# Kernel optimization log

Hardware: AMD Instinct MI355X
Metric: run time of the kernel (lower is better)

## Reference

```python
import jax, jax.numpy as jnp
import numpy as np

T, DIM, AH, HID, E = 2048, 1024, 2048, 1024, 8
N_HEADS, HEAD_DIM = 16, 128
N_GROUPS, TOPK_GROUPS, TOPK = 4, 2, 1
ROUTE_SCALE = 1.0


def rmsnorm(x, w, eps=1e-6):
    xf = x.astype(jnp.float32)
    var = jnp.mean(xf * xf, axis=-1, keepdims=True)
    return (xf * jax.lax.rsqrt(var + eps)).astype(x.dtype) * w


def setup_inputs() -> dict:
    key = jax.random.key(0)
    ks = jax.random.split(key, 12)

    def xavier(k, fan_in, fan_out, gain=1.0):
        lim = gain * np.sqrt(6.0 / (fan_in + fan_out))
        return jax.random.uniform(k, (fan_in, fan_out), minval=-lim, maxval=lim, dtype=jnp.float32)

    return {
        "x": jax.random.normal(ks[0], (T, DIM), dtype=jnp.float32),
        "x_projected": jax.random.normal(ks[1], (T, AH), dtype=jnp.float32),
        "attn_norm_w": jnp.ones((AH,), dtype=jnp.float32),
        # stored as [in, out] (transposed vs torch Linear)
        "wq": 0.02 * jax.random.normal(ks[2], (AH, N_HEADS * HEAD_DIM), dtype=jnp.float32),
        "bq": jnp.zeros((N_HEADS * HEAD_DIM,), dtype=jnp.float32),
        "wk": 0.02 * jax.random.normal(ks[3], (AH, N_HEADS * HEAD_DIM), dtype=jnp.float32),
        "bk": jnp.zeros((N_HEADS * HEAD_DIM,), dtype=jnp.float32),
        "q_norm_w": jnp.ones((HEAD_DIM,), dtype=jnp.float32),
        "k_norm_w": jnp.ones((HEAD_DIM,), dtype=jnp.float32),
        "w1": xavier(ks[4], DIM, HID),
        "b1": jnp.zeros((HID,), dtype=jnp.float32),
        "w2": xavier(ks[5], HID, HID),
        "b2": jnp.zeros((HID,), dtype=jnp.float32),
        "w3": xavier(ks[6], HID, E, gain=0.1),
        "b3": jnp.zeros((E,), dtype=jnp.float32),
    }


def reference(x, x_projected, attn_norm_w, wq, bq, wk, bk, q_norm_w, k_norm_w,
              w1, b1, w2, b2, w3, b3):
    t = x.shape[0]
    # ---- attention probe (torch.no_grad -> stop_gradient) ----
    xn = rmsnorm(x_projected, attn_norm_w)                      # [T, AH]
    q = (xn @ wq + bq).reshape(t, N_HEADS, HEAD_DIM)
    k = (xn @ wk + bk).reshape(t, N_HEADS, HEAD_DIM)
    q = rmsnorm(q, q_norm_w)
    k = rmsnorm(k, k_norm_w)
    scores = jnp.einsum('qhd,khd->hqk', q, k) / np.float32(np.sqrt(HEAD_DIM))
    probs = jax.nn.softmax(scores, axis=-1)                     # [H, T, T]
    # sum over query axis, mean over heads -> attention received per token
    importance = jax.lax.stop_gradient(probs.sum(axis=1).mean(axis=0))  # [T]

    # ---- router MLP (eval mode: dropout = identity) ----
    h = jax.nn.gelu(x @ w1 + b1, approximate=False)
    h = jax.nn.gelu(h @ w2 + b2, approximate=False)
    logits = h @ w3 + b3                                        # [T, E]
    r_scores = jax.nn.softmax(logits, axis=-1)

    # ---- grouped top-k (group-limited top-1 routing) ----
    sg = r_scores.reshape(t, N_GROUPS, E // N_GROUPS)
    group_scores = sg.max(axis=-1)                              # [T, G]
    _, gidx = jax.lax.top_k(group_scores, TOPK_GROUPS)          # [T, kg]
    mask = jnp.zeros((t, N_GROUPS), dtype=bool).at[jnp.arange(t)[:, None], gidx].set(True)
    masked = jnp.where(mask[:, :, None], sg, -jnp.inf).reshape(t, E)
    _, idx = jax.lax.top_k(masked, TOPK)                        # [T, 1]
    weights = jnp.take_along_axis(r_scores, idx, axis=1) * ROUTE_SCALE  # [T, 1]
    return weights, idx, importance
```

## Files before the change

### kernel.cpp

```cpp
#include <hip/hip_runtime.h>

#define T_TOK 2048
#define DIMX  1024
#define AHX   2048
#define HIDX  1024
#define NEXP  8
#define NHEAD 16
#define HD    128

typedef short bf16x8 __attribute__((ext_vector_type(8)));
typedef float f32x4  __attribute__((ext_vector_type(4)));

__device__ __forceinline__ unsigned short f2bf(float f){
  unsigned int u = __builtin_bit_cast(unsigned int, f);
  u += 0x7FFFu + ((u >> 16) & 1u);
  return (unsigned short)(u >> 16);
}
__device__ __forceinline__ float bf2f(unsigned short h){
  unsigned int u = ((unsigned int)h) << 16;
  return __builtin_bit_cast(float, u);
}
__device__ __forceinline__ float gelu_exact(float x){
  return 0.5f * x * (1.0f + erff(x * 0.70710678118654752440f));
}
__device__ __forceinline__ void gload16(const unsigned short* g, unsigned short* l){
  __builtin_amdgcn_global_load_lds((const __attribute__((address_space(1))) unsigned int*)g,
                                   (__attribute__((address_space(3))) unsigned int*)l, 16, 0, 0);
}

__global__ __launch_bounds__(256) void k_prep(const float* __restrict__ x,
                                              unsigned short* __restrict__ xh,
                                              unsigned short* __restrict__ xl,
                                              const float* __restrict__ xproj,
                                              const float* __restrict__ anw,
                                              unsigned short* __restrict__ xn){
  int bx = blockIdx.x, t = threadIdx.x;
  if (bx < 8192){
    int i = bx * 256 + t;
    float v = x[i];
    unsigned short h = f2bf(v);
    xh[i] = h;
    xl[i] = f2bf(v - bf2f(h));
    return;
  }
  int row = bx - 8192;
  const float* p = xproj + (size_t)row * AHX;
  float v[8];
  *(float4*)&v[0] = *(const float4*)(p + t * 8);
  *(float4*)&v[4] = *(const float4*)(p + t * 8 + 4);
  float s = 0.f;
  #pragma unroll
  for (int i = 0; i < 8; i++) s += v[i] * v[i];
  #pragma unroll
  for (int m = 1; m < 64; m <<= 1) s += __shfl_xor(s, m);
  __shared__ float ps[4];
  if ((t & 63) == 0) ps[t >> 6] = s;
  __syncthreads();
  float tot = ps[0] + ps[1] + ps[2] + ps[3];
  float rs = rsqrtf(tot * (1.0f / AHX) + 1e-6f);
  #pragma unroll
  for (int i = 0; i < 8; i++)
    xn[(size_t)row * AHX + t * 8 + i] = f2bf(v[i] * rs * anw[t * 8 + i]);
}

__global__ void k_transpose_qk(const float* __restrict__ wq, const float* __restrict__ wk,
                               unsigned short* __restrict__ out){
  const float* in = blockIdx.z ? wk : wq;
  unsigned short* o = out + (size_t)blockIdx.z * AHX * AHX;
  __shared__ float tile[32][33];
  int bx = blockIdx.x * 32, by = blockIdx.y * 32;
  int tx = threadIdx.x, ty = threadIdx.y;
  #pragma unroll
  for (int i = 0; i < 32; i += 8)
    tile[ty + i][tx] = in[(size_t)(by + ty + i) * AHX + bx + tx];
  __syncthreads();
  #pragma unroll
  for (int i = 0; i < 32; i += 8)
    o[(size_t)(bx + ty + i) * AHX + by + tx] = f2bf(tile[tx][ty + i]);
}

__global__ void k_transpose_w12(const float* __restrict__ w1, const float* __restrict__ w2,
                                unsigned short* __restrict__ w1h, unsigned short* __restrict__ w1l,
                                unsigned short* __restrict__ w2h, unsigned short* __restrict__ w2l){
  const float* in = blockIdx.z ? w2 : w1;
  unsigned short* oh = blockIdx.z ? w2h : w1h;
  unsigned short* ol = blockIdx.z ? w2l : w1l;
  __shared__ float tile[32][33];
  int bx = blockIdx.x * 32, by = blockIdx.y * 32;
  int tx = threadIdx.x, ty = threadIdx.y;
  #pragma unroll
  for (int i = 0; i < 32; i += 8)
    tile[ty + i][tx] = in[(size_t)(by + ty + i) * HIDX + bx + tx];
  __syncthreads();
  #pragma unroll
  for (int i = 0; i < 32; i += 8){
    float v = tile[tx][ty + i];
    unsigned short h = f2bf(v);
    size_t o = (size_t)(bx + ty + i) * DIMX + by + tx;
    oh[o] = h;
    ol[o] = f2bf(v - bf2f(h));
  }
}

__global__ __launch_bounds__(256) void k_gemm_qk(
    const unsigned short* __restrict__ A, const unsigned short* __restrict__ B,
    const float* __restrict__ bq, const float* __restrict__ bk,
    const float* __restrict__ qnw, const float* __restrict__ knw,
    unsigned short* __restrict__ Qnn, unsigned short* __restrict__ Knn, int K)
{
  __shared__ __align__(16) unsigned short sA[2][128 * 64];
  __shared__ __align__(16) unsigned short sB[2][128 * 64];
  __shared__ float sums[128][2];
  int tid = threadIdx.x;
  int bm = blockIdx.y * 128;
  int bnB = blockIdx.x * 128;
  int w = tid >> 6, l = tid & 63;
  int wm = (w >> 1) * 64, wn = (w & 1) * 64;
  int lhi = l >> 4, llo = l & 15;
  int srow = l >> 3;
  int scol = ((l & 7) ^ srow) * 8;
  int swz = llo & 7;

  const unsigned short* pA = &A[(size_t)(bm + w * 32 + srow) * K + scol];
  const unsigned short* pB = &B[(size_t)(bnB + w * 32 + srow) * K + scol];

  f32x4 acc[4][4] = {};

  #pragma unroll
  for (int i = 0; i < 4; i++){
    gload16(pA + (size_t)i * 8 * K, &sA[0][(w * 32 + i * 8) * 64]);
    gload16(pB + (size_t)i * 8 * K, &sB[0][(w * 32 + i * 8) * 64]);
  }
  __syncthreads();

  int cur = 0;
  for (int k0 = 0; k0 < K; k0 += 64){
    if (k0 + 64 < K){
      #pragma unroll
      for (int i = 0; i < 4; i++){
        gload16(pA + (size_t)i * 8 * K + k0 + 64, &sA[cur ^ 1][(w * 32 + i * 8) * 64]);
        gload16(pB + (size_t)i * 8 * K + k0 + 64, &sB[cur ^ 1][(w * 32 + i * 8) * 64]);
      }
    }
    bf16x8 af[2][4], bfr[2][4];
    #pragma unroll
    for (int kk = 0; kk < 2; kk++){
      int ca = ((kk * 4 + lhi) ^ swz) * 8;
      #pragma unroll
      for (int m = 0; m < 4; m++){
        af[kk][m]  = *(const bf16x8*)&sA[cur][(wm + m * 16 + llo) * 64 + ca];
        bfr[kk][m] = *(const bf16x8*)&sB[cur][(wn + m * 16 + llo) * 64 + ca];
      }
    }
    #pragma unroll
    for (int kk = 0; kk < 2; kk++)
      #pragma unroll
      for (int m = 0; m < 4; m++)
        #pragma unroll
        for (int n = 0; n < 4; n++)
          acc[m][n] = __builtin_amdgcn_mfma_f32_16x16x32_bf16(af[kk][m], bfr[kk][n], acc[m][n], 0, 0, 0);
    __syncthreads();
    cur ^= 1;
  }

  bool isq = blockIdx.x < 16;
  const float* bias = isq ? bq : bk;
  const float* nw   = isq ? qnw : knw;
  unsigned short* outp = isq ? Qnn : Knn;
  int hcol0 = (blockIdx.x & 15) * 128;

  #pragma unroll
  for (int n = 0; n < 4; n++){
    float bv = bias[hcol0 + wn + n * 16 + llo];
    #pragma unroll
    for (int m = 0; m < 4; m++)
      #pragma unroll
      for (int j = 0; j < 4; j++) acc[m][n][j] += bv;
  }
  #pragma unroll
  for (int m = 0; m < 4; m++)
    #pragma unroll
    for (int j = 0; j < 4; j++){
      float p = 0.f;
      #pragma unroll
      for (int n = 0; n < 4; n++) p += acc[m][n][j] * acc[m][n][j];
      p += __shfl_xor(p, 1); p += __shfl_xor(p, 2);
      p += __shfl_xor(p, 4); p += __shfl_xor(p, 8);
      if (llo == 0) sums[wm + m * 16 + lhi * 4 + j][w & 1] = p;
    }
  __syncthreads();
  #pragma unroll
  for (int m = 0; m < 4; m++)
    #pragma unroll
    for (int j = 0; j < 4; j++){
      int row = wm + m * 16 + lhi * 4 + j;
      float rs = rsqrtf((sums[row][0] + sums[row][1]) * (1.0f / HD) + 1e-6f);
      #pragma unroll
      for (int n = 0; n < 4; n++){
        int col = wn + n * 16 + llo;
        outp[(size_t)(bm + row) * AHX + hcol0 + col] = f2bf(acc[m][n][j] * rs * nw[col]);
      }
    }
}

template<int EPI>
__global__ __launch_bounds__(256) void k_gemm_mlp(
    const unsigned short* __restrict__ Ah_, const unsigned short* __restrict__ Al_,
    const unsigned short* __restrict__ Bh_, const unsigned short* __restrict__ Bl_,
    const float* __restrict__ bias,
    float* __restrict__ Cf, unsigned short* __restrict__ Ch, unsigned short* __restrict__ Cl,
    int N, int K)
{
  __shared__ __align__(16) unsigned short sAh[2][64 * 64], sAl[2][64 * 64];
  __shared__ __align__(16) unsigned short sBh[2][64 * 64], sBl[2][64 * 64];
  int tid = threadIdx.x;
  int bm = blockIdx.y * 64, bn = blockIdx.x * 64;
  int w = tid >> 6, l = tid & 63;
  int wm = (w >> 1) * 32, wn = (w & 1) * 32;
  int lhi = l >> 4, llo = l & 15;
  int srow = l >> 3;
  int scol = ((l & 7) ^ srow) * 8;
  int swz = llo & 7;

  const unsigned short* pAh = &Ah_[(size_t)(bm + w * 8 + srow) * K + scol];
  const unsigned short* pAl = &Al_[(size_t)(bm + w * 8 + srow) * K + scol];
  const unsigned short* pBh = &Bh_[(size_t)(bn + w * 8 + srow) * K + scol];
  const unsigned short* pBl = &Bl_[(size_t)(bn + w * 8 + srow) * K + scol];

  f32x4 acc[2][2] = {};

  auto stage = [&](int buf, int k0){
    #pragma unroll
    for (int i = 0; i < 2; i++){
      int rb = (i * 32 + w * 8) * 64;
      gload16(pAh + (size_t)i * 32 * K + k0, &sAh[buf][rb]);
      gload16(pAl + (size_t)i * 32 * K + k0, &sAl[buf][rb]);
      gload16(pBh + (size_t)i * 32 * K + k0, &sBh[buf][rb]);
      gload16(pBl + (size_t)i * 32 * K + k0, &sBl[buf][rb]);
    }
  };

  stage(0, 0);
  __syncthreads();

  int cur = 0;
  for (int k0 = 0; k0 < K; k0 += 64){
    if (k0 + 64 < K) stage(cur ^ 1, k0 + 64);
    bf16x8 ah[2][2], al[2][2], bh[2][2], bl[2][2];
    #pragma unroll
    for (int kk = 0; kk < 2; kk++){
      int ca = ((kk * 4 + lhi) ^ swz) * 8;
      #pragma unroll
      for (int m = 0; m < 2; m++){
        ah[kk][m] = *(const bf16x8*)&sAh[cur][(wm + m * 16 + llo) * 64 + ca];
        al[kk][m] = *(const bf16x8*)&sAl[cur][(wm + m * 16 + llo) * 64 + ca];
        bh[kk][m] = *(const bf16x8*)&sBh[cur][(wn + m * 16 + llo) * 64 + ca];
        bl[kk][m] = *(const bf16x8*)&sBl[cur][(wn + m * 16 + llo) * 64 + ca];
      }
    }
    #pragma unroll
    for (int kk = 0; kk < 2; kk++)
      #pragma unroll
      for (int m = 0; m < 2; m++)
        #pragma unroll
        for (int n = 0; n < 2; n++){
          acc[m][n] = __builtin_amdgcn_mfma_f32_16x16x32_bf16(ah[kk][m], bh[kk][n], acc[m][n], 0, 0, 0);
          acc[m][n] = __builtin_amdgcn_mfma_f32_16x16x32_bf16(ah[kk][m], bl[kk][n], acc[m][n], 0, 0, 0);
          acc[m][n] = __builtin_amdgcn_mfma_f32_16x16x32_bf16(al[kk][m], bh[kk][n], acc[m][n], 0, 0, 0);
        }
    __syncthreads();
    cur ^= 1;
  }

  #pragma unroll
  for (int m = 0; m < 2; m++)
    #pragma unroll
    for (int n = 0; n < 2; n++){
      int col = bn + wn + n * 16 + llo;
      float bv = bias[col];
      #pragma unroll
      for (int j = 0; j < 4; j++){
        int row = bm + wm + m * 16 + lhi * 4 + j;
        float v = acc[m][n][j] + bv;
        size_t off = (size_t)row * N + col;
        if constexpr (EPI == 1){
          float g = gelu_exact(v);
          unsigned short hh = f2bf(g);
          Ch[off] = hh;
          Cl[off] = f2bf(g - bf2f(hh));
        } else {
          Cf[off] = gelu_exact(v);
        }
      }
    }
}

__global__ __launch_bounds__(256) void k_z(const unsigned short* __restrict__ Qn,
                                           const unsigned short* __restrict__ Kn,
                                           float* __restrict__ zpart){
  __shared__ __align__(16) unsigned short sK[2][128 * 128];
  int h = blockIdx.y;
  int qb = blockIdx.x * 128;
  int tid = threadIdx.x, w = tid >> 6, l = tid & 63;
  int lhi = l >> 4, llo = l & 15;
  int wq = qb + w * 32;
  const float scale = 0.08838834764831845f;

  auto stageK = [&](int buf, int kt){
    #pragma unroll
    for (int i = 0; i < 8; i++){
      int rb = i * 16 + w * 4;
      int r = rb + (l >> 4);
      int c = ((l & 15) * 8) ^ ((r & 7) << 3);
      gload16(&Kn[(size_t)(kt + r) * AHX + h * HD + c], &sK[buf][rb * 128]);
    }
  };

  bf16x8 qf[2][4];
  #pragma unroll
  for (int m = 0; m < 2; m++)
    #pragma unroll
    for (int kk = 0; kk < 4; kk++)
      qf[m][kk] = *(const bf16x8*)&Qn[(size_t)(wq + m * 16 + llo) * AHX + h * HD + kk * 32 + lhi * 8];

  float rz[2][4] = {};
  int kt0 = blockIdx.z * 256;

  stageK(0, kt0);
  __syncthreads();

  #pragma unroll
  for (int t = 0; t < 2; t++){
    if (t == 0) stageK(1, kt0 + 128);
    f32x4 acc[2][8] = {};
    #pragma unroll
    for (int n = 0; n < 8; n++){
      int row = n * 16 + llo;
      #pragma unroll
      for (int kk = 0; kk < 4; kk++){
        bf16x8 kf = *(const bf16x8*)&sK[t][row * 128 + ((kk * 32 + lhi * 8) ^ ((llo & 7) << 3))];
        acc[0][n] = __builtin_amdgcn_mfma_f32_16x16x32_bf16(qf[0][kk], kf, acc[0][n], 0, 0, 0);
        acc[1][n] = __builtin_amdgcn_mfma_f32_16x16x32_bf16(qf[1][kk], kf, acc[1][n], 0, 0, 0);
      }
    }
    #pragma unroll
    for (int m = 0; m < 2; m++)
      #pragma unroll
      for (int j = 0; j < 4; j++){
        float s = 0.f;
        #pragma unroll
        for (int n = 0; n < 8; n++) s += __expf(acc[m][n][j] * scale);
        rz[m][j] += s;
      }
    if (t == 0) __syncthreads();
  }
  #pragma unroll
  for (int m = 0; m < 2; m++)
    #pragma unroll
    for (int j = 0; j < 4; j++){
      float s = rz[m][j];
      s += __shfl_xor(s, 1); s += __shfl_xor(s, 2);
      s += __shfl_xor(s, 4); s += __shfl_xor(s, 8);
      if (llo == 0){
        int row = wq + m * 16 + lhi * 4 + j;
        zpart[(size_t)blockIdx.z * (NHEAD * T_TOK) + h * T_TOK + row] = s;
      }
    }
}

__global__ void k_rc(const float* __restrict__ zpart, float* __restrict__ rc){
  int i = blockIdx.x * 256 + threadIdx.x;
  float s = 0.f;
  #pragma unroll
  for (int p = 0; p < 8; p++) s += zpart[p * (NHEAD * T_TOK) + i];
  rc[i] = 1.0f / ((float)NHEAD * s);
}

__global__ __launch_bounds__(256) void k_imp(const unsigned short* __restrict__ Qn,
                                             const unsigned short* __restrict__ Kn,
                                             const float* __restrict__ rc,
                                             float* __restrict__ imp_part){
  __shared__ __align__(16) unsigned short sK[2][128 * 128];
  __shared__ float simp[4][128];
  int h = blockIdx.y;
  int qb = blockIdx.x * 128;
  int kt0 = blockIdx.z * 256;
  int tid = threadIdx.x, w = tid >> 6, l = tid & 63;
  int lhi = l >> 4, llo = l & 15;
  int wq = qb + w * 32;
  const float scale = 0.08838834764831845f;

  auto stageK = [&](int buf, int kt){
    #pragma unroll
    for (int i = 0; i < 8; i++){
      int rb = i * 16 + w * 4;
      int r = rb + (l >> 4);
      int c = ((l & 15) * 8) ^ ((r & 7) << 3);
      gload16(&Kn[(size_t)(kt + r) * AHX + h * HD + c], &sK[buf][rb * 128]);
    }
  };

  bf16x8 qf[2][4];
  float rcv[2][4];
  #pragma unroll
  for (int m = 0; m < 2; m++)
    #pragma unroll
    for (int kk = 0; kk < 4; kk++)
      qf[m][kk] = *(const bf16x8*)&Qn[(size_t)(wq + m * 16 + llo) * AHX + h * HD + kk * 32 + lhi * 8];
  #pragma unroll
  for (int m = 0; m < 2; m++)
    #pragma unroll
    for (int j = 0; j < 4; j++)
      rcv[m][j] = rc[h * T_TOK + wq + m * 16 + lhi * 4 + j];

  stageK(0, kt0);
  __syncthreads();

  #pragma unroll
  for (int t = 0; t < 2; t++){
    if (t == 0) stageK(1, kt0 + 128);
    f32x4 acc[2][8] = {};
    #pragma unroll
    for (int n = 0; n < 8; n++){
      int row = n * 16 + llo;
      #pragma unroll
      for (int kk = 0; kk < 4; kk++){
        bf16x8 kf = *(const bf16x8*)&sK[t][row * 128 + ((kk * 32 + lhi * 8) ^ ((llo & 7) << 3))];
        acc[0][n] = __builtin_amdgcn_mfma_f32_16x16x32_bf16(qf[0][kk], kf, acc[0][n], 0, 0, 0);
        acc[1][n] = __builtin_amdgcn_mfma_f32_16x16x32_bf16(qf[1][kk], kf, acc[1][n], 0, 0, 0);
      }
    }
    #pragma unroll
    for (int n = 0; n < 8; n++){
      float s = 0.f;
      #pragma unroll
      for (int m = 0; m < 2; m++)
        #pragma unroll
        for (int j = 0; j < 4; j++)
          s += __expf(acc[m][j / 4 * 0 + n][j] * 0.f + acc[m][n][j] * scale) * 0.f + __expf(acc[m][n][j] * scale) * rcv[m][j];
      s += __shfl_xor(s, 16);
      s += __shfl_xor(s, 32);
      if (l < 16) simp[w][n * 16 + l] = s;
    }
    __syncthreads();
    if (tid < 128){
      float tot = simp[0][tid] + simp[1][tid] + simp[2][tid] + simp[3][tid];
      imp_part[((size_t)blockIdx.x * NHEAD + h) * T_TOK + kt0 + t * 128 + tid] = tot;
    }
    if (t == 0) __syncthreads();
  }
}

__global__ __launch_bounds__(256) void k_final(const float* __restrict__ imp_part,
                                               const float* __restrict__ h2,
                                               const float* __restrict__ w3,
                                               const float* __restrict__ b3,
                                               float* __restrict__ out){
  if (blockIdx.x < 8){
    int col = blockIdx.x * 256 + threadIdx.x;
    float s = 0.f;
    for (int r = 0; r < 256; r++) s += imp_part[(size_t)r * T_TOK + col];
    out[2 * T_TOK + col] = s;
    return;
  }
  int t = (blockIdx.x - 8) * 4 + (threadIdx.x >> 6);
  int l = threadIdx.x & 63;
  const float* hp = h2 + (size_t)t * HIDX;
  float acc[NEXP] = {};
  for (int i = l; i < HIDX; i += 64){
    float hv = hp[i];
    const float* wr = w3 + (size_t)i * NEXP;
    #pragma unroll
    for (int e = 0; e < NEXP; e++) acc[e] = fmaf(hv, wr[e], acc[e]);
  }
  #pragma unroll
  for (int mk = 1; mk < 64; mk <<= 1)
    #pragma unroll
    for (int e = 0; e < NEXP; e++) acc[e] += __shfl_xor(acc[e], mk);
  if (l == 0){
    float lg[NEXP], mx = -__builtin_inff();
    #pragma unroll
    for (int e = 0; e < NEXP; e++){ lg[e] = acc[e] + b3[e]; mx = fmaxf(mx, lg[e]); }
    float Z = 0.f, p[NEXP];
    #pragma unroll
    for (int e = 0; e < NEXP; e++){ p[e] = expf(lg[e] - mx); Z += p[e]; }
    float invZ = 1.0f / Z;
    #pragma unroll
    for (int e = 0; e < NEXP; e++) p[e] *= invZ;
    float gs[4];
    #pragma unroll
    for (int g = 0; g < 4; g++) gs[g] = fmaxf(p[2 * g], p[2 * g + 1]);
    int g1 = 0;
    #pragma unroll
    for (int g = 1; g < 4; g++) if (gs[g] > gs[g1]) g1 = g;
    int g2 = -1; float g2v = -__builtin_inff();
    #pragma unroll
    for (int g = 0; g < 4; g++) if (g != g1 && gs[g] > g2v){ g2v = gs[g]; g2 = g; }
    int best = 0; float bv = -__builtin_inff();
    #pragma unroll
    for (int e = 0; e < NEXP; e++){
      int g = e >> 1;
      if ((g == g1 || g == g2) && p[e] > bv){ bv = p[e]; best = e; }
    }
    out[t]         = bv;
    out[T_TOK + t] = (float)best;
  }
}

extern "C" void kernel_launch(void* const* d_in, const int* in_sizes, int n_in,
                              void* d_out, int out_size, void* d_ws, size_t ws_size,
                              hipStream_t stream){
  const float* x     = (const float*)d_in[0];
  const float* xproj = (const float*)d_in[1];
  const float* anw   = (const float*)d_in[2];
  const float* wq    = (const float*)d_in[3];
  const float* bq    = (const float*)d_in[4];
  const float* wk    = (const float*)d_in[5];
  const float* bk    = (const float*)d_in[6];
  const float* qnw   = (const float*)d_in[7];
  const float* knw   = (const float*)d_in[8];
  const float* w1    = (const float*)d_in[9];
  const float* b1    = (const float*)d_in[10];
  const float* w2    = (const float*)d_in[11];
  const float* b2    = (const float*)d_in[12];
  const float* w3    = (const float*)d_in[13];
  const float* b3    = (const float*)d_in[14];
  float* out = (float*)d_out;

  char* ws = (char*)d_ws;
  const size_t MB = 1024 * 1024;
  unsigned short* xn   = (unsigned short*)(ws);
  unsigned short* wqkT = (unsigned short*)(ws + 8 * MB);
  unsigned short* Qnn  = (unsigned short*)(ws + 24 * MB);
  unsigned short* Knn  = (unsigned short*)(ws + 32 * MB);
  float* zpart         = (float*)(ws + 40 * MB);
  float* rc            = (float*)(ws + 41 * MB);
  float* imp_part      = (float*)(ws + 42 * MB);
  unsigned short* xh   = (unsigned short*)(ws + 44 * MB);
  unsigned short* xl   = (unsigned short*)(ws + 48 * MB);
  unsigned short* w1Th = (unsigned short*)(ws + 52 * MB);
  unsigned short* w1Tl = (unsigned short*)(ws + 54 * MB);
  unsigned short* w2Th = (unsigned short*)(ws + 56 * MB);
  unsigned short* w2Tl = (unsigned short*)(ws + 58 * MB);
  unsigned short* h1h  = (unsigned short*)(ws + 60 * MB);
  unsigned short* h1l  = (unsigned short*)(ws + 64 * MB);
  float* h2            = (float*)(ws + 68 * MB);

  dim3 tb(32, 8);
  k_prep<<<8192 + T_TOK, 256, 0, stream>>>(x, xh, xl, xproj, anw, xn);
  k_transpose_qk<<<dim3(AHX / 32, AHX / 32, 2), tb, 0, stream>>>(wq, wk, wqkT);

  k_gemm_qk<<<dim3(32, 16), 256, 0, stream>>>(xn, wqkT, bq, bk, qnw, knw, Qnn, Knn, AHX);

  k_transpose_w12<<<dim3(HIDX / 32, DIMX / 32, 2), tb, 0, stream>>>(w1, w2, w1Th, w1Tl, w2Th, w2Tl);

  k_z<<<dim3(16, NHEAD, 8), 256, 0, stream>>>(Qnn, Knn, zpart);
  k_rc<<<(NHEAD * T_TOK) / 256, 256, 0, stream>>>(zpart, rc);
  k_imp<<<dim3(16, NHEAD, 8), 256, 0, stream>>>(Qnn, Knn, rc, imp_part);

  k_gemm_mlp<1><<<dim3(HIDX / 64, T_TOK / 64), 256, 0, stream>>>(
      xh, xl, w1Th, w1Tl, b1, nullptr, h1h, h1l, HIDX, DIMX);
  k_gemm_mlp<2><<<dim3(HIDX / 64, T_TOK / 64), 256, 0, stream>>>(
      h1h, h1l, w2Th, w2Tl, b2, h2, nullptr, nullptr, HIDX, HIDX);

  k_final<<<8 + T_TOK / 4, 256, 0, stream>>>(imp_part, h2, w3, b3, out);

  (void)in_sizes; (void)n_in; (void)out_size; (void)ws_size;
}
```

Measured before the change: 194.5 us.

## Merge prep/transpose kernels, fold rc into imp, use 512-thread blocks for attention GEMMs

Merges the prep and both weight-transpose kernels into one launch, and folds the k_rc normalization into k_imp so it reads zpart directly. It also doubles block size to 512 threads for the QK projection, z and importance kernels, so each wave holds a smaller tile and fewer accumulators. The intent is to cut launch count and raise occupancy and latency hiding. The cost is less register reuse per wave, redundant zpart reads in k_imp, and an extra barrier per iteration.

```diff
diff --git a/kernel.cpp b/kernel.cpp
--- a/kernel.cpp
+++ b/kernel.cpp
@@ -8,128 +8,136 @@
 #define NHEAD 16
 #define HD    128
 
+typedef unsigned short us;
 typedef short bf16x8 __attribute__((ext_vector_type(8)));
 typedef float f32x4  __attribute__((ext_vector_type(4)));
 
-__device__ __forceinline__ unsigned short f2bf(float f){
+__device__ __forceinline__ us f2bf(float f){
   unsigned int u = __builtin_bit_cast(unsigned int, f);
   u += 0x7FFFu + ((u >> 16) & 1u);
-  return (unsigned short)(u >> 16);
-}
-__device__ __forceinline__ float bf2f(unsigned short h){
+  return (us)(u >> 16);
+}
+__device__ __forceinline__ float bf2f(us h){
   unsigned int u = ((unsigned int)h) << 16;
   return __builtin_bit_cast(float, u);
 }
 __device__ __forceinline__ float gelu_exact(float x){
   return 0.5f * x * (1.0f + erff(x * 0.70710678118654752440f));
 }
-__device__ __forceinline__ void gload16(const unsigned short* g, unsigned short* l){
+__device__ __forceinline__ void gload16(const us* g, us* l){
   __builtin_amdgcn_global_load_lds((const __attribute__((address_space(1))) unsigned int*)g,
                                    (__attribute__((address_space(3))) unsigned int*)l, 16, 0, 0);
 }
 
-__global__ __launch_bounds__(256) void k_prep(const float* __restrict__ x,
-                                              unsigned short* __restrict__ xh,
-                                              unsigned short* __restrict__ xl,
-                                              const float* __restrict__ xproj,
-                                              const float* __restrict__ anw,
-                                              unsigned short* __restrict__ xn){
+__global__ __launch_bounds__(256) void k_pre(const float* __restrict__ x,
+                                             us* __restrict__ xh, us* __restrict__ xl,
+                                             const float* __restrict__ xproj,
+                                             const float* __restrict__ anw,
+                                             us* __restrict__ xn,
+                                             const float* __restrict__ wq,
+                                             const float* __restrict__ wk,
+                                             us* __restrict__ wqkT,
+                                             const float* __restrict__ w1,
+                                             const float* __restrict__ w2,
+                                             us* __restrict__ w1h, us* __restrict__ w1l,
+                                             us* __restrict__ w2h, us* __restrict__ w2l){
+  __shared__ float tile[32][33];
+  __shared__ float ps[4];
   int bx = blockIdx.x, t = threadIdx.x;
   if (bx < 8192){
     int i = bx * 256 + t;
     float v = x[i];
-    unsigned short h = f2bf(v);
+    us h = f2bf(v);
     xh[i] = h;
     xl[i] = f2bf(v - bf2f(h));
     return;
   }
-  int row = bx - 8192;
-  const float* p = xproj + (size_t)row * AHX;
-  float v[8];
-  *(float4*)&v[0] = *(const float4*)(p + t * 8);
-  *(float4*)&v[4] = *(const float4*)(p + t * 8 + 4);
-  float s = 0.f;
-  #pragma unroll
-  for (int i = 0; i < 8; i++) s += v[i] * v[i];
-  #pragma unroll
-  for (int m = 1; m < 64; m <<= 1) s += __shfl_xor(s, m);
-  __shared__ float ps[4];
-  if ((t & 63) == 0) ps[t >> 6] = s;
-  __syncthreads();
-  float tot = ps[0] + ps[1] + ps[2] + ps[3];
-  float rs = rsqrtf(tot * (1.0f / AHX) + 1e-6f);
-  #pragma unroll
-  for (int i = 0; i < 8; i++)
-    xn[(size_t)row * AHX + t * 8 + i] = f2bf(v[i] * rs * anw[t * 8 + i]);
-}
-
-__global__ void k_transpose_qk(const float* __restrict__ wq, const float* __restrict__ wk,
-                               unsigned short* __restrict__ out){
-  const float* in = blockIdx.z ? wk : wq;
-  unsigned short* o = out + (size_t)blockIdx.z * AHX * AHX;
-  __shared__ float tile[32][33];
-  int bx = blockIdx.x * 32, by = blockIdx.y * 32;
-  int tx = threadIdx.x, ty = threadIdx.y;
-  #pragma unroll
-  for (int i = 0; i < 32; i += 8)
-    tile[ty + i][tx] = in[(size_t)(by + ty + i) * AHX + bx + tx];
-  __syncthreads();
-  #pragma unroll
-  for (int i = 0; i < 32; i += 8)
-    o[(size_t)(bx + ty + i) * AHX + by + tx] = f2bf(tile[tx][ty + i]);
-}
-
-__global__ void k_transpose_w12(const float* __restrict__ w1, const float* __restrict__ w2,
-                                unsigned short* __restrict__ w1h, unsigned short* __restrict__ w1l,
-                                unsigned short* __restrict__ w2h, unsigned short* __restrict__ w2l){
-  const float* in = blockIdx.z ? w2 : w1;
-  unsigned short* oh = blockIdx.z ? w2h : w1h;
-  unsigned short* ol = blockIdx.z ? w2l : w1l;
-  __shared__ float tile[32][33];
-  int bx = blockIdx.x * 32, by = blockIdx.y * 32;
-  int tx = threadIdx.x, ty = threadIdx.y;
-  #pragma unroll
-  for (int i = 0; i < 32; i += 8)
-    tile[ty + i][tx] = in[(size_t)(by + ty + i) * HIDX + bx + tx];
-  __syncthreads();
-  #pragma unroll
-  for (int i = 0; i < 32; i += 8){
-    float v = tile[tx][ty + i];
-    unsigned short h = f2bf(v);
-    size_t o = (size_t)(bx + ty + i) * DIMX + by + tx;
-    oh[o] = h;
-    ol[o] = f2bf(v - bf2f(h));
-  }
-}
-
-__global__ __launch_bounds__(256) void k_gemm_qk(
-    const unsigned short* __restrict__ A, const unsigned short* __restrict__ B,
+  if (bx < 10240){
+    int row = bx - 8192;
+    const float* p = xproj + (size_t)row * AHX;
+    float v[8];
+    *(float4*)&v[0] = *(const float4*)(p + t * 8);
+    *(float4*)&v[4] = *(const float4*)(p + t * 8 + 4);
+    float s = 0.f;
+    #pragma unroll
+    for (int i = 0; i < 8; i++) s += v[i] * v[i];
+    #pragma unroll
+    for (int m = 1; m < 64; m <<= 1) s += __shfl_xor(s, m);
+    if ((t & 63) == 0) ps[t >> 6] = s;
+    __syncthreads();
+    float tot = ps[0] + ps[1] + ps[2] + ps[3];
+    float rs = rsqrtf(tot * (1.0f / AHX) + 1e-6f);
+    #pragma unroll
+    for (int i = 0; i < 8; i++)
+      xn[(size_t)row * AHX + t * 8 + i] = f2bf(v[i] * rs * anw[t * 8 + i]);
+    return;
+  }
+  int tx = t & 31, ty = t >> 5;
+  if (bx < 18432){
+    int sub = bx - 10240;
+    const float* in = (sub >> 12) ? wk : wq;
+    us* o = wqkT + (size_t)(sub >> 12) * AHX * AHX;
+    int rem = sub & 4095;
+    int tbx = (rem & 63) * 32, tby = (rem >> 6) * 32;
+    #pragma unroll
+    for (int i = 0; i < 32; i += 8)
+      tile[ty + i][tx] = in[(size_t)(tby + ty + i) * AHX + tbx + tx];
+    __syncthreads();
+    #pragma unroll
+    for (int i = 0; i < 32; i += 8)
+      o[(size_t)(tbx + ty + i) * AHX + tby + tx] = f2bf(tile[tx][ty + i]);
+    return;
+  }
+  {
+    int sub = bx - 18432;
+    const float* in = (sub >> 10) ? w2 : w1;
+    us* oh = (sub >> 10) ? w2h : w1h;
+    us* ol = (sub >> 10) ? w2l : w1l;
+    int rem = sub & 1023;
+    int tbx = (rem & 31) * 32, tby = (rem >> 5) * 32;
+    #pragma unroll
+    for (int i = 0; i < 32; i += 8)
+      tile[ty + i][tx] = in[(size_t)(tby + ty + i) * HIDX + tbx + tx];
+    __syncthreads();
+    #pragma unroll
+    for (int i = 0; i < 32; i += 8){
+      float v = tile[tx][ty + i];
+      us h = f2bf(v);
+      size_t o = (size_t)(tbx + ty + i) * DIMX + tby + tx;
+      oh[o] = h;
+      ol[o] = f2bf(v - bf2f(h));
+    }
+  }
+}
+
+__global__ __launch_bounds__(512) void k_gemm_qk(
+    const us* __restrict__ A, const us* __restrict__ B,
     const float* __restrict__ bq, const float* __restrict__ bk,
     const float* __restrict__ qnw, const float* __restrict__ knw,
-    unsigned short* __restrict__ Qnn, unsigned short* __restrict__ Knn, int K)
+    us* __restrict__ Qnn, us* __restrict__ Knn, int K)
 {
-  __shared__ __align__(16) unsigned short sA[2][128 * 64];
-  __shared__ __align__(16) unsigned short sB[2][128 * 64];
-  __shared__ float sums[128][2];
+  __shared__ __align__(16) us sA[2][128 * 64];
+  __shared__ __align__(16) us sB[2][128 * 64];
+  __shared__ float sums[128][4];
   int tid = threadIdx.x;
   int bm = blockIdx.y * 128;
   int bnB = blockIdx.x * 128;
   int w = tid >> 6, l = tid & 63;
-  int wm = (w >> 1) * 64, wn = (w & 1) * 64;
+  int wm = (w >> 2) * 64, wn = (w & 3) * 32;
   int lhi = l >> 4, llo = l & 15;
   int srow = l >> 3;
   int scol = ((l & 7) ^ srow) * 8;
   int swz = llo & 7;
 
-  const unsigned short* pA = &A[(size_t)(bm + w * 32 + srow) * K + scol];
-  const unsigned short* pB = &B[(size_t)(bnB + w * 32 + srow) * K + scol];
-
-  f32x4 acc[4][4] = {};
-
-  #pragma unroll
-  for (int i = 0; i < 4; i++){
-    gload16(pA + (size_t)i * 8 * K, &sA[0][(w * 32 + i * 8) * 64]);
-    gload16(pB + (size_t)i * 8 * K, &sB[0][(w * 32 + i * 8) * 64]);
+  const us* pA = &A[(size_t)(bm + w * 16 + srow) * K + scol];
+  const us* pB = &B[(size_t)(bnB + w * 16 + srow) * K + scol];
+
+  f32x4 acc[4][2] = {};
+
+  #pragma unroll
+  for (int i = 0; i < 2; i++){
+    gload16(pA + (size_t)i * 8 * K, &sA[0][(w * 16 + i * 8) * 64]);
+    gload16(pB + (size_t)i * 8 * K, &sB[0][(w * 16 + i * 8) * 64]);
   }
   __syncthreads();
 
@@ -137,27 +145,28 @@
   for (int k0 = 0; k0 < K; k0 += 64){
     if (k0 + 64 < K){
       #pragma unroll
-      for (int i = 0; i < 4; i++){
-        gload16(pA + (size_t)i * 8 * K + k0 + 64, &sA[cur ^ 1][(w * 32 + i * 8) * 64]);
-        gload16(pB + (size_t)i * 8 * K + k0 + 64, &sB[cur ^ 1][(w * 32 + i * 8) * 64]);
+      for (int i = 0; i < 2; i++){
+        gload16(pA + (size_t)i * 8 * K + k0 + 64, &sA[cur ^ 1][(w * 16 + i * 8) * 64]);
+        gload16(pB + (size_t)i * 8 * K + k0 + 64, &sB[cur ^ 1][(w * 16 + i * 8) * 64]);
       }
     }
-    bf16x8 af[2][4], bfr[2][4];
+    bf16x8 af[2][4], bfr[2][2];
     #pragma unroll
     for (int kk = 0; kk < 2; kk++){
       int ca = ((kk * 4 + lhi) ^ swz) * 8;
       #pragma unroll
-      for (int m = 0; m < 4; m++){
-        af[kk][m]  = *(const bf16x8*)&sA[cur][(wm + m * 16 + llo) * 64 + ca];
-        bfr[kk][m] = *(const bf16x8*)&sB[cur][(wn + m * 16 + llo) * 64 + ca];
-      }
+      for (int m = 0; m < 4; m++)
+        af[kk][m] = *(const bf16x8*)&sA[cur][(wm + m * 16 + llo) * 64 + ca];
+      #pragma unroll
+      for (int n = 0; n < 2; n++)
+        bfr[kk][n] = *(const bf16x8*)&sB[cur][(wn + n * 16 + llo) * 64 + ca];
     }
     #pragma unroll
     for (int kk = 0; kk < 2; kk++)
       #pragma unroll
       for (int m = 0; m < 4; m++)
         #pragma unroll
-        for (int n = 0; n < 4; n++)
+        for (int n = 0; n < 2; n++)
           acc[m][n] = __builtin_amdgcn_mfma_f32_16x16x32_bf16(af[kk][m], bfr[kk][n], acc[m][n], 0, 0, 0);
     __syncthreads();
     cur ^= 1;
@@ -166,11 +175,11 @@
   bool isq = blockIdx.x < 16;
   const float* bias = isq ? bq : bk;
   const float* nw   = isq ? qnw : knw;
-  unsigned short* outp = isq ? Qnn : Knn;
+  us* outp = isq ? Qnn : Knn;
   int hcol0 = (blockIdx.x & 15) * 128;
 
   #pragma unroll
-  for (int n = 0; n < 4; n++){
+  for (int n = 0; n < 2; n++){
     float bv = bias[hcol0 + wn + n * 16 + llo];
     #pragma unroll
     for (int m = 0; m < 4; m++)
@@ -183,10 +192,10 @@
     for (int j = 0; j < 4; j++){
       float p = 0.f;
       #pragma unroll
-      for (int n = 0; n < 4; n++) p += acc[m][n][j] * acc[m][n][j];
+      for (int n = 0; n < 2; n++) p += acc[m][n][j] * acc[m][n][j];
       p += __shfl_xor(p, 1); p += __shfl_xor(p, 2);
       p += __shfl_xor(p, 4); p += __shfl_xor(p, 8);
-      if (llo == 0) sums[wm + m * 16 + lhi * 4 + j][w & 1] = p;
+      if (llo == 0) sums[wm + m * 16 + lhi * 4 + j][w & 3] = p;
     }
   __syncthreads();
   #pragma unroll
@@ -194,9 +203,9 @@
     #pragma unroll
     for (int j = 0; j < 4; j++){
       int row = wm + m * 16 + lhi * 4 + j;
-      float rs = rsqrtf((sums[row][0] + sums[row][1]) * (1.0f / HD) + 1e-6f);
-      #pragma unroll
-      for (int n = 0; n < 4; n++){
+      float rs = rsqrtf((sums[row][0] + sums[row][1] + sums[row][2] + sums[row][3]) * (1.0f / HD) + 1e-6f);
+      #pragma unroll
+      for (int n = 0; n < 2; n++){
         int col = wn + n * 16 + llo;
         outp[(size_t)(bm + row) * AHX + hcol0 + col] = f2bf(acc[m][n][j] * rs * nw[col]);
       }
@@ -205,14 +214,14 @@
 
 template<int EPI>
 __global__ __launch_bounds__(256) void k_gemm_mlp(
-    const unsigned short* __restrict__ Ah_, const unsigned short* __restrict__ Al_,
-    const unsigned short* __restrict__ Bh_, const unsigned short* __restrict__ Bl_,
+    const us* __restrict__ Ah_, const us* __restrict__ Al_,
+    const us* __restrict__ Bh_, const us* __restrict__ Bl_,
     const float* __restrict__ bias,
-    float* __restrict__ Cf, unsigned short* __restrict__ Ch, unsigned short* __restrict__ Cl,
+    float* __restrict__ Cf, us* __restrict__ Ch, us* __restrict__ Cl,
     int N, int K)
 {
-  __shared__ __align__(16) unsigned short sAh[2][64 * 64], sAl[2][64 * 64];
-  __shared__ __align__(16) unsigned short sBh[2][64 * 64], sBl[2][64 * 64];
+  __shared__ __align__(16) us sAh[2][64 * 64], sAl[2][64 * 64];
+  __shared__ __align__(16) us sBh[2][64 * 64], sBl[2][64 * 64];
   int tid = threadIdx.x;
   int bm = blockIdx.y * 64, bn = blockIdx.x * 64;
   int w = tid >> 6, l = tid & 63;
@@ -222,10 +231,10 @@
   int scol = ((l & 7) ^ srow) * 8;
   int swz = llo & 7;
 
-  const unsigned short* pAh = &Ah_[(size_t)(bm + w * 8 + srow) * K + scol];
-  const unsigned short* pAl = &Al_[(size_t)(bm + w * 8 + srow) * K + scol];
-  const unsigned short* pBh = &Bh_[(size_t)(bn + w * 8 + srow) * K + scol];
-  const unsigned short* pBl = &Bl_[(size_t)(bn + w * 8 + srow) * K + scol];
+  const us* pAh = &Ah_[(size_t)(bm + w * 8 + srow) * K + scol];
+  const us* pAl = &Al_[(size_t)(bm + w * 8 + srow) * K + scol];
+  const us* pBh = &Bh_[(size_t)(bn + w * 8 + srow) * K + scol];
+  const us* pBl = &Bl_[(size_t)(bn + w * 8 + srow) * K + scol];
 
   f32x4 acc[2][2] = {};
 
@@ -285,7 +294,7 @@
         size_t off = (size_t)row * N + col;
         if constexpr (EPI == 1){
           float g = gelu_exact(v);
-          unsigned short hh = f2bf(g);
+          us hh = f2bf(g);
           Ch[off] = hh;
           Cl[off] = f2bf(g - bf2f(hh));
         } else {
@@ -295,35 +304,33 @@
     }
 }
 
-__global__ __launch_bounds__(256) void k_z(const unsigned short* __restrict__ Qn,
-                                           const unsigned short* __restrict__ Kn,
+__global__ __launch_bounds__(512) void k_z(const us* __restrict__ Qn,
+                                           const us* __restrict__ Kn,
                                            float* __restrict__ zpart){
-  __shared__ __align__(16) unsigned short sK[2][128 * 128];
+  __shared__ __align__(16) us sK[2][128 * 128];
   int h = blockIdx.y;
   int qb = blockIdx.x * 128;
   int tid = threadIdx.x, w = tid >> 6, l = tid & 63;
   int lhi = l >> 4, llo = l & 15;
-  int wq = qb + w * 32;
+  int wq = qb + w * 16;
   const float scale = 0.08838834764831845f;
 
   auto stageK = [&](int buf, int kt){
     #pragma unroll
-    for (int i = 0; i < 8; i++){
-      int rb = i * 16 + w * 4;
-      int r = rb + (l >> 4);
-      int c = ((l & 15) * 8) ^ ((r & 7) << 3);
+    for (int i = 0; i < 4; i++){
+      int rb = w * 16 + i * 4;
+      int r = rb + lhi;
+      int c = ((llo ^ (r & 7))) * 8;
       gload16(&Kn[(size_t)(kt + r) * AHX + h * HD + c], &sK[buf][rb * 128]);
     }
   };
 
-  bf16x8 qf[2][4];
-  #pragma unroll
-  for (int m = 0; m < 2; m++)
-    #pragma unroll
-    for (int kk = 0; kk < 4; kk++)
-      qf[m][kk] = *(const bf16x8*)&Qn[(size_t)(wq + m * 16 + llo) * AHX + h * HD + kk * 32 + lhi * 8];
-
-  float rz[2][4] = {};
+  bf16x8 qf[4];
+  #pragma unroll
+  for (int kk = 0; kk < 4; kk++)
+    qf[kk] = *(const bf16x8*)&Qn[(size_t)(wq + llo) * AHX + h * HD + kk * 32 + lhi * 8];
+
+  float rz[4] = {};
   int kt0 = blockIdx.z * 256;
 
   stageK(0, kt0);
@@ -332,86 +339,74 @@
   #pragma unroll
   for (int t = 0; t < 2; t++){
     if (t == 0) stageK(1, kt0 + 128);
-    f32x4 acc[2][8] = {};
+    f32x4 acc[8] = {};
     #pragma unroll
     for (int n = 0; n < 8; n++){
       int row = n * 16 + llo;
       #pragma unroll
       for (int kk = 0; kk < 4; kk++){
         bf16x8 kf = *(const bf16x8*)&sK[t][row * 128 + ((kk * 32 + lhi * 8) ^ ((llo & 7) << 3))];
-        acc[0][n] = __builtin_amdgcn_mfma_f32_16x16x32_bf16(qf[0][kk], kf, acc[0][n], 0, 0, 0);
-        acc[1][n] = __builtin_amdgcn_mfma_f32_16x16x32_bf16(qf[1][kk], kf, acc[1][n], 0, 0, 0);
+        acc[n] = __builtin_amdgcn_mfma_f32_16x16x32_bf16(qf[kk], kf, acc[n], 0, 0, 0);
       }
     }
     #pragma unroll
-    for (int m = 0; m < 2; m++)
-      #pragma unroll
-      for (int j = 0; j < 4; j++){
-        float s = 0.f;
-        #pragma unroll
-        for (int n = 0; n < 8; n++) s += __expf(acc[m][n][j] * scale);
-        rz[m][j] += s;
-      }
+    for (int j = 0; j < 4; j++){
+      float s = 0.f;
+      #pragma unroll
+      for (int n = 0; n < 8; n++) s += __expf(acc[n][j] * scale);
+      rz[j] += s;
+    }
     if (t == 0) __syncthreads();
   }
   #pragma unroll
-  for (int m = 0; m < 2; m++)
-    #pragma unroll
-    for (int j = 0; j < 4; j++){
-      float s = rz[m][j];
-      s += __shfl_xor(s, 1); s += __shfl_xor(s, 2);
-      s += __shfl_xor(s, 4); s += __shfl_xor(s, 8);
-      if (llo == 0){
-        int row = wq + m * 16 + lhi * 4 + j;
-        zpart[(size_t)blockIdx.z * (NHEAD * T_TOK) + h * T_TOK + row] = s;
-      }
-    }
-}
-
-__global__ void k_rc(const float* __restrict__ zpart, float* __restrict__ rc){
-  int i = blockIdx.x * 256 + threadIdx.x;
-  float s = 0.f;
-  #pragma unroll
-  for (int p = 0; p < 8; p++) s += zpart[p * (NHEAD * T_TOK) + i];
-  rc[i] = 1.0f / ((float)NHEAD * s);
-}
-
-__global__ __launch_bounds__(256) void k_imp(const unsigned short* __restrict__ Qn,
-                                             const unsigned short* __restrict__ Kn,
-                                             const float* __restrict__ rc,
+  for (int j = 0; j < 4; j++){
+    float s = rz[j];
+    s += __shfl_xor(s, 1); s += __shfl_xor(s, 2);
+    s += __shfl_xor(s, 4); s += __shfl_xor(s, 8);
+    if (llo == 0){
+      int row = wq + lhi * 4 + j;
+      zpart[(size_t)blockIdx.z * (NHEAD * T_TOK) + h * T_TOK + row] = s;
+    }
+  }
+}
+
+__global__ __launch_bounds__(512) void k_imp(const us* __restrict__ Qn,
+                                             const us* __restrict__ Kn,
+                                             const float* __restrict__ zpart,
                                              float* __restrict__ imp_part){
-  __shared__ __align__(16) unsigned short sK[2][128 * 128];
-  __shared__ float simp[4][128];
+  __shared__ __align__(16) us sK[2][128 * 128];
+  __shared__ float simp[8][128];
   int h = blockIdx.y;
   int qb = blockIdx.x * 128;
   int kt0 = blockIdx.z * 256;
   int tid = threadIdx.x, w = tid >> 6, l = tid & 63;
   int lhi = l >> 4, llo = l & 15;
-  int wq = qb + w * 32;
+  int wq = qb + w * 16;
   const float scale = 0.08838834764831845f;
 
   auto stageK = [&](int buf, int kt){
     #pragma unroll
-    for (int i = 0; i < 8; i++){
-      int rb = i * 16 + w * 4;
-      int r = rb + (l >> 4);
-      int c = ((l & 15) * 8) ^ ((r & 7) << 3);
+    for (int i = 0; i < 4; i++){
+      int rb = w * 16 + i * 4;
+      int r = rb + lhi;
+      int c = ((llo ^ (r & 7))) * 8;
       gload16(&Kn[(size_t)(kt + r) * AHX + h * HD + c], &sK[buf][rb * 128]);
     }
   };
 
-  bf16x8 qf[2][4];
-  float rcv[2][4];
-  #pragma unroll
-  for (int m = 0; m < 2; m++)
-    #pragma unroll
-    for (int kk = 0; kk < 4; kk++)
-      qf[m][kk] = *(const bf16x8*)&Qn[(size_t)(wq + m * 16 + llo) * AHX + h * HD + kk * 32 + lhi * 8];
-  #pragma unroll
-  for (int m = 0; m < 2; m++)
-    #pragma unroll
-    for (int j = 0; j < 4; j++)
-      rcv[m][j] = rc[h * T_TOK + wq + m * 16 + lhi * 4 + j];
+  bf16x8 qf[4];
+  float rcv[4];
+  #pragma unroll
+  for (int kk = 0; kk < 4; kk++)
+    qf[kk] = *(const bf16x8*)&Qn[(size_t)(wq + llo) * AHX + h * HD + kk * 32 + lhi * 8];
+  #pragma unroll
+  for (int j = 0; j < 4; j++){
+    int row = wq + lhi * 4 + j;
+    float zs = 0.f;
+    #pragma unroll
+    for (int p = 0; p < 8; p++) zs += zpart[(size_t)p * (NHEAD * T_TOK) + h * T_TOK + row];
+    rcv[j] = 1.0f / ((float)NHEAD * zs);
+  }
 
   stageK(0, kt0);
   __syncthreads();
@@ -419,35 +414,34 @@
   #pragma unroll
   for (int t = 0; t < 2; t++){
     if (t == 0) stageK(1, kt0 + 128);
-    f32x4 acc[2][8] = {};
+    f32x4 acc[8] = {};
     #pragma unroll
     for (int n = 0; n < 8; n++){
       int row = n * 16 + llo;
       #pragma unroll
       for (int kk = 0; kk < 4; kk++){
         bf16x8 kf = *(const bf16x8*)&sK[t][row * 128 + ((kk * 32 + lhi * 8) ^ ((llo & 7) << 3))];
-        acc[0][n] = __builtin_amdgcn_mfma_f32_16x16x32_bf16(qf[0][kk], kf, acc[0][n], 0, 0, 0);
-        acc[1][n] = __builtin_amdgcn_mfma_f32_16x16x32_bf16(qf[1][kk], kf, acc[1][n], 0, 0, 0);
+        acc[n] = __builtin_amdgcn_mfma_f32_16x16x32_bf16(qf[kk], kf, acc[n], 0, 0, 0);
       }
     }
     #pragma unroll
     for (int n = 0; n < 8; n++){
       float s = 0.f;
       #pragma unroll
-      for (int m = 0; m < 2; m++)
-        #pragma unroll
-        for (int j = 0; j < 4; j++)
-          s += __expf(acc[m][j / 4 * 0 + n][j] * 0.f + acc[m][n][j] * scale) * 0.f + __expf(acc[m][n][j] * scale) * rcv[m][j];
+      for (int j = 0; j < 4; j++)
+        s += __expf(acc[n][j] * scale) * rcv[j];
       s += __shfl_xor(s, 16);
       s += __shfl_xor(s, 32);
       if (l < 16) simp[w][n * 16 + l] = s;
     }
     __syncthreads();
     if (tid < 128){
-      float tot = simp[0][tid] + simp[1][tid] + simp[2][tid] + simp[3][tid];
+      float tot = 0.f;
+      #pragma unroll
+      for (int ww = 0; ww < 8; ww++) tot += simp[ww][tid];
       imp_part[((size_t)blockIdx.x * NHEAD + h) * T_TOK + kt0 + t * 128 + tid] = tot;
     }
-    if (t == 0) __syncthreads();
+    __syncthreads();
   }
 }
 
@@ -529,34 +523,29 @@
 
   char* ws = (char*)d_ws;
   const size_t MB = 1024 * 1024;
-  unsigned short* xn   = (unsigned short*)(ws);
-  unsigned short* wqkT = (unsigned short*)(ws + 8 * MB);
-  unsigned short* Qnn  = (unsigned short*)(ws + 24 * MB);
-  unsigned short* Knn  = (unsigned short*)(ws + 32 * MB);
-  float* zpart         = (float*)(ws + 40 * MB);
-  float* rc            = (float*)(ws + 41 * MB);
-  float* imp_part      = (float*)(ws + 42 * MB);
-  unsigned short* xh   = (unsigned short*)(ws + 44 * MB);
-  unsigned short* xl   = (unsigned short*)(ws + 48 * MB);
-  unsigned short* w1Th = (unsigned short*)(ws + 52 * MB);
-  unsigned short* w1Tl = (unsigned short*)(ws + 54 * MB);
-  unsigned short* w2Th = (unsigned short*)(ws + 56 * MB);
-  unsigned short* w2Tl = (unsigned short*)(ws + 58 * MB);
-  unsigned short* h1h  = (unsigned short*)(ws + 60 * MB);
-  unsigned short* h1l  = (unsigned short*)(ws + 64 * MB);
-  float* h2            = (float*)(ws + 68 * MB);
-
-  dim3 tb(32, 8);
-  k_prep<<<8192 + T_TOK, 256, 0, stream>>>(x, xh, xl, xproj, anw, xn);
-  k_transpose_qk<<<dim3(AHX / 32, AHX / 32, 2), tb, 0, stream>>>(wq, wk, wqkT);
-
-  k_gemm_qk<<<dim3(32, 16), 256, 0, stream>>>(xn, wqkT, bq, bk, qnw, knw, Qnn, Knn, AHX);
-
-  k_transpose_w12<<<dim3(HIDX / 32, DIMX / 32, 2), tb, 0, stream>>>(w1, w2, w1Th, w1Tl, w2Th, w2Tl);
-
-  k_z<<<dim3(16, NHEAD, 8), 256, 0, stream>>>(Qnn, Knn, zpart);
-  k_rc<<<(NHEAD * T_TOK) / 256, 256, 0, stream>>>(zpart, rc);
-  k_imp<<<dim3(16, NHEAD, 8), 256, 0, stream>>>(Qnn, Knn, rc, imp_part);
+  us* xn      = (us*)(ws);
+  us* wqkT    = (us*)(ws + 8 * MB);
+  us* Qnn     = (us*)(ws + 24 * MB);
+  us* Knn     = (us*)(ws + 32 * MB);
+  float* zpart    = (float*)(ws + 40 * MB);
+  float* imp_part = (float*)(ws + 42 * MB);
+  us* xh      = (us*)(ws + 44 * MB);
+  us* xl      = (us*)(ws + 48 * MB);
+  us* w1Th    = (us*)(ws + 52 * MB);
+  us* w1Tl    = (us*)(ws + 54 * MB);
+  us* w2Th    = (us*)(ws + 56 * MB);
+  us* w2Tl    = (us*)(ws + 58 * MB);
+  us* h1h     = (us*)(ws + 60 * MB);
+  us* h1l     = (us*)(ws + 64 * MB);
+  float* h2   = (float*)(ws + 68 * MB);
+
+  k_pre<<<20480, 256, 0, stream>>>(x, xh, xl, xproj, anw, xn,
+                                   wq, wk, wqkT, w1, w2, w1Th, w1Tl, w2Th, w2Tl);
+
+  k_gemm_qk<<<dim3(32, 16), 512, 0, stream>>>(xn, wqkT, bq, bk, qnw, knw, Qnn, Knn, AHX);
+
+  k_z<<<dim3(16, NHEAD, 8), 512, 0, stream>>>(Qnn, Knn, zpart);
+  k_imp<<<dim3(16, NHEAD, 8), 512, 0, stream>>>(Qnn, Knn, zpart, imp_part);
 
   k_gemm_mlp<1><<<dim3(HIDX / 64, T_TOK / 64), 256, 0, stream>>>(
       xh, xl, w1Th, w1Tl, b1, nullptr, h1h, h1l, HIDX, DIMX);
```

Result: faster. 181.7 us (-6.6%).
